# Performance work log

Hardware: AMD Instinct MI355X
Metric: run time of the kernel (lower is better)

## Reference

```python
import jax, jax.numpy as jnp
import numpy as np

EPS = 1e-12  # matches torch F.normalize eps and utils.get_diagonal threshold


def _geteig(feats, K):
    # feats: [B, C, H, W]
    B, C, H, W = feats.shape
    nH, nW = H // 4, W // 4
    # bilinear, align_corners=False (half-pixel centers) == jax.image.resize 'bilinear'
    f = jax.image.resize(feats, (B, C, nH, nW), method='bilinear')
    f = f.reshape(B, C, nH * nW).transpose(0, 2, 1)  # [B, N, C]
    norm = jnp.linalg.norm(f, axis=-1, keepdims=True)
    f = f / jnp.maximum(norm, EPS)  # L2-normalize per pixel

    def per_sample(x):  # x: [N, C]
        Wm = x @ x.T                       # cosine similarity [N, N]
        Wm = Wm * (Wm > 0)                 # keep positive affinities
        Wm = Wm / Wm.max()
        Wm = jax.lax.stop_gradient(Wm)     # original detaches before eigsh
        d = Wm.sum(axis=1)                 # degree (row sums), as in utils.get_diagonal
        d = jnp.where(d < EPS, 1.0, d)
        inv_sqrt = 1.0 / jnp.sqrt(d)
        L = jnp.diag(d) - Wm               # unnormalized Laplacian
        # generalized problem L v = lam D v  <=>  eigh of D^-1/2 L D^-1/2
        Ln = inv_sqrt[:, None] * L * inv_sqrt[None, :]
        Ln = 0.5 * (Ln + Ln.T)             # enforce symmetry for stability
        evals = jnp.linalg.eigh(Ln)[0]     # ascending
        return evals[:K]                   # K smallest (eigsh sigma=0, which='LM')

    return jax.vmap(per_sample)(f)  # [B, K]


def setup_inputs() -> dict:
    key = jax.random.key(0)
    feats = jax.random.normal(key, (8, 3, 160, 160), dtype=jnp.float32)
    return {"feats": feats, "K": 10}


def reference(feats, K):
    lan1 = _geteig(feats[:, :1], K)    # channel 0 -> [B, K]
    lan2 = _geteig(feats[:, 1:2], K)   # channel 1 -> [B, K]
    # NOTE: faithful to original bug: feats[:2:3] slices the BATCH dim -> [1, C, H, W]
    lan3 = _geteig(feats[:2:3], K)     # [1, K], broadcasts in the MSE below
    loss = jnp.mean((lan1 - lan2) ** 2)
    loss = loss + jnp.mean((lan1 - lan3) ** 2)
    loss = loss + jnp.mean((lan2 - lan3) ** 2)
    return loss * 5
```

## Files before the change

### kernel.cpp

```cpp
#include <hip/hip_runtime.h>
#include <math.h>

#define N16 1600
#define M 32
#define XSZ 51200
#define BIS_IT 28
#define EPSF 1e-12f


__device__ void taps1d(int o, int* lo, int* hi, float* wsum, float w[8]) {
  int l = 4 * o - 2, h = 4 * o + 5;
  if (l < 0) l = 0;
  if (h > 159) h = 159;
  float c = 4.f * o + 1.5f, s = 0.f;
  for (int x = l; x <= h; ++x) {
    float ww = 1.f - fabsf((float)x - c) * 0.25f;
    w[x - l] = ww;
    s += ww;
  }
  *lo = l; *hi = h; *wsum = s;
}

__global__ void __launch_bounds__(256)
k_resize(const float* __restrict__ in, float* __restrict__ rz) {
  const int bx = blockIdx.x, t = threadIdx.x;
  int map = bx / 7;
  int o = (bx % 7) * 256 + t;
  if (o >= N16) return;
  int oy = o / 40, ox = o % 40;
  int ly, hy, lx, hx; float sy, sx; float wy[8], wx[8];
  taps1d(oy, &ly, &hy, &sy, wy);
  taps1d(ox, &lx, &hx, &sx, wx);
  const float* src = in + (size_t)map * 160 * 160;
  float acc = 0.f;
  for (int y = ly; y <= hy; ++y) {
    float a = 0.f;
    const float* row = src + y * 160;
    for (int x = lx; x <= hx; ++x) a += wx[x - lx] * row[x];
    acc += wy[y - ly] * a;
  }
  rz[map * N16 + o] = acc / (sy * sx);
}

__global__ void __launch_bounds__(256)
k_prep(const float* __restrict__ rz, float* __restrict__ F,
       int* __restrict__ flags) {
  __shared__ int sp[256];
  __shared__ int sn[256];
  const int bx = blockIdx.x, t = threadIdx.x;
  if (bx < 16) {
    int b = bx >> 1, c = bx & 1;
    const float* m = rz + (b * 3 + c) * N16;
    int cp = 0, cn = 0;
    for (int o = t; o < N16; o += 256) {
      float v = m[o];
      cp += (v > 0.f);
      cn += (v < 0.f);
    }
    sp[t] = cp; sn[t] = cn;
    __syncthreads();
    for (int s = 128; s > 0; s >>= 1) {
      if (t < s) { sp[t] += sp[t + s]; sn[t] += sn[t + s]; }
      __syncthreads();
    }
    if (t == 0) flags[bx] = (sp[0] == 0 || sn[0] == 0) ? 1 : 0;
  } else {
    int n = (bx - 16) * 256 + t;
    if (n < N16) {
      float x = rz[n], y = rz[N16 + n], z = rz[2 * N16 + n];
      float nrm = sqrtf(x * x + y * y + z * z);
      float s = 1.f / fmaxf(nrm, EPSF);
      F[n * 3 + 0] = x * s;
      F[n * 3 + 1] = y * s;
      F[n * 3 + 2] = z * s;
    }
  }
}

__global__ void __launch_bounds__(256)
k_degree(const float* __restrict__ F, float* __restrict__ R,
         float* __restrict__ G4f, float* __restrict__ X0) {
  __shared__ float Fl[4800];
  __shared__ float red[256];
  const int bx = blockIdx.x, t = threadIdx.x;
  for (int s = t; s < 4800; s += 256) Fl[s] = F[s];
  __syncthreads();
  int rl = t >> 4, jt = t & 15;
  int i = bx * 16 + rl;
  float fx = Fl[i * 3], fy = Fl[i * 3 + 1], fz = Fl[i * 3 + 2];
  float s = 0.f;
#pragma unroll 8
  for (int j = jt; j < N16; j += 16) {
    float w = fx * Fl[j * 3] + fy * Fl[j * 3 + 1] + fz * Fl[j * 3 + 2];
    if (w > 0.f) s += w;
  }
  red[t] = s;
  __syncthreads();
  for (int st = 8; st > 0; st >>= 1) {
    if (jt < st) red[t] += red[t + st];
    __syncthreads();
  }
  if (jt == 0) {
    float d = red[t];
    if (d < EPSF) d = 1.f;
    float r = rsqrtf(d);
    R[i] = r;
    G4f[i * 4 + 0] = r * fx;
    G4f[i * 4 + 1] = r * fy;
    G4f[i * 4 + 2] = r * fz;
    G4f[i * 4 + 3] = 0.f;
  }
  for (int e = t; e < 512; e += 256) {
    int n = bx * 16 + (e >> 5);
    int k = e & 31;
    unsigned u = ((unsigned)n * 2654435761u) ^ ((unsigned)k * 0x9E3779B9u);
    u = u * 1664525u + 1013904223u;
    u ^= u >> 16; u *= 2246822519u; u ^= u >> 13;
    X0[n * M + k] = ((float)(u >> 8) * (1.f / 8388608.f)) - 1.f;
  }
}

__global__ void __launch_bounds__(256)
k_mv(const float* __restrict__ F, const float4* __restrict__ G4,
     const float* __restrict__ R, const float* __restrict__ Xin,
     float* __restrict__ Xout) {
  __shared__ float Ws[2][544];
  __shared__ float XsT[2][1088];
  __shared__ float Red[16 * 136];
  const int bx = blockIdx.x, t = threadIdx.x;
  const int ig = bx >> 1, kh = bx & 1;
  const int i0 = ig * 8, kbase = kh * 16;
  const int rg = t & 3, kg = (t >> 2) & 3, jg = t >> 4;
  const int sj = t >> 2, sq = t & 3;
  const int wil = t & 7, wjg = t >> 3;
  const float fx = F[(i0 + wil) * 3 + 0];
  const float fy = F[(i0 + wil) * 3 + 1];
  const float fz = F[(i0 + wil) * 3 + 2];

  float acc[2][4];
#pragma unroll
  for (int r = 0; r < 2; ++r)
#pragma unroll
    for (int kk = 0; kk < 4; ++kk) acc[r][kk] = 0.f;

  {
    float4 xs = ((const float4*)Xin)[(size_t)sj * 8 + kh * 4 + sq];
    XsT[0][(sq * 4 + 0) * 68 + sj] = xs.x;
    XsT[0][(sq * 4 + 1) * 68 + sj] = xs.y;
    XsT[0][(sq * 4 + 2) * 68 + sj] = xs.z;
    XsT[0][(sq * 4 + 3) * 68 + sj] = xs.w;
#pragma unroll
    for (int q = 0; q < 2; ++q) {
      float4 g = G4[wjg + 32 * q];
      Ws[0][wil * 68 + wjg + 32 * q] =
          fmaxf(fx * g.x + fy * g.y + fz * g.z, 0.f);
    }
  }
  __syncthreads();

  for (int c = 0; c < 25; ++c) {
    const int cur = c & 1, nxt = cur ^ 1;
    float4 xs = {0.f, 0.f, 0.f, 0.f};
    float4 ga[2];
    if (c < 24) {
      const int jb = (c + 1) * 64;
      xs = ((const float4*)Xin)[(size_t)(jb + sj) * 8 + kh * 4 + sq];
#pragma unroll
      for (int q = 0; q < 2; ++q) ga[q] = G4[jb + wjg + 32 * q];
    }
    {
      const int jq = jg * 4;
      float4 wv[2], xv[4];
#pragma unroll
      for (int r = 0; r < 2; ++r)
        wv[r] = *(const float4*)&Ws[cur][(rg * 2 + r) * 68 + jq];
#pragma unroll
      for (int kk = 0; kk < 4; ++kk)
        xv[kk] = *(const float4*)&XsT[cur][(kg * 4 + kk) * 68 + jq];
#pragma unroll
      for (int r = 0; r < 2; ++r)
#pragma unroll
        for (int kk = 0; kk < 4; ++kk)
          acc[r][kk] += wv[r].x * xv[kk].x + wv[r].y * xv[kk].y +
                        wv[r].z * xv[kk].z + wv[r].w * xv[kk].w;
    }
    if (c < 24) {
      XsT[nxt][(sq * 4 + 0) * 68 + sj] = xs.x;
      XsT[nxt][(sq * 4 + 1) * 68 + sj] = xs.y;
      XsT[nxt][(sq * 4 + 2) * 68 + sj] = xs.z;
      XsT[nxt][(sq * 4 + 3) * 68 + sj] = xs.w;
#pragma unroll
      for (int q = 0; q < 2; ++q)
        Ws[nxt][wil * 68 + wjg + 32 * q] =
            fmaxf(fx * ga[q].x + fy * ga[q].y + fz * ga[q].z, 0.f);
    }
    __syncthreads();
  }

#pragma unroll
  for (int r = 0; r < 2; ++r)
#pragma unroll
    for (int kk = 0; kk < 4; ++kk)
      Red[jg * 136 + (rg * 2 + r) * 16 + (kg * 4 + kk)] = acc[r][kk];
  __syncthreads();
  if (t < 128) {
    const int il = t >> 4, kl = t & 15;
    float sv = 0.f;
#pragma unroll
    for (int g = 0; g < 16; ++g) sv += Red[g * 136 + il * 16 + kl];
    const int gi = i0 + il, gk = kbase + kl;
    Xout[(size_t)gi * 32 + gk] =
        0.5f * Xin[(size_t)gi * 32 + gk] + 0.5f * R[gi] * sv;
  }
}

__global__ void __launch_bounds__(256)
k_gram(const float* __restrict__ Xa, const float* __restrict__ Xb,
       float* __restrict__ GPp) {
  __shared__ float sA[2048];
  __shared__ float sB[2048];
  const int bx = blockIdx.x, t = threadIdx.x;
  float acc[4] = {0.f, 0.f, 0.f, 0.f};
  for (int c = 0; c < 5; ++c) {
    const int j0 = bx * 320 + c * 64;
    __syncthreads();
    for (int s = t; s < 2048; s += 256) {
      sA[s] = Xa[(size_t)j0 * 32 + s];
      sB[s] = Xb[(size_t)j0 * 32 + s];
    }
    __syncthreads();
#pragma unroll
    for (int s = 0; s < 4; ++s) {
      int e = s * 256 + t;
      int a = e >> 5, b = e & 31;
      float sum = 0.f;
#pragma unroll 8
      for (int jl = 0; jl < 64; ++jl) sum += sA[jl * 32 + a] * sB[jl * 32 + b];
      acc[s] += sum;
    }
  }
#pragma unroll
  for (int s = 0; s < 4; ++s) GPp[(size_t)bx * 1024 + s * 256 + t] = acc[s];
}

__global__ void __launch_bounds__(256)
k_apply(const float* __restrict__ GPp, const float* __restrict__ Xin,
        float* __restrict__ Xout) {
  __shared__ float Gm[32 * 33];
  const int bx = blockIdx.x, t = threadIdx.x;
#pragma unroll
  for (int u = 0; u < 4; ++u) {
    int e = t + u * 256;
    float g = 0.f;
#pragma unroll
    for (int p = 0; p < 5; ++p) g += GPp[p * 1024 + e];
    Gm[(e >> 5) * 33 + (e & 31)] = g;
  }
  const int r = t >> 5, l = t & 31;
  const int row = bx * 8 + r;
  float x = Xin[(size_t)row * M + l];
  __syncthreads();
  if (t < 64) {
    for (int k = 0; k < 32; ++k) {
      if (t == k) Gm[k * 33 + k] = sqrtf(fmaxf(Gm[k * 33 + k], 1e-30f));
      float piv = Gm[k * 33 + k];
      if (t > k && t < 32) Gm[t * 33 + k] /= piv;
#pragma unroll
      for (int u = 0; u < 16; ++u) {
        int e = t + u * 64;
        int i = e >> 5, j = e & 31;
        if (i > k && j > k && j <= i)
          Gm[i * 33 + j] -= Gm[i * 33 + k] * Gm[j * 33 + k];
      }
    }
  }
  __syncthreads();
  const int half = t & 32;
  float y = 0.f;
  for (int k = 0; k < 32; ++k) {
    float gkl = Gm[k * 33 + l];
    float contrib = (l < k) ? y * gkl : 0.f;
#pragma unroll
    for (int o = 16; o; o >>= 1) contrib += __shfl_xor(contrib, o, 64);
    float xk = __shfl(x, half + k, 64);
    float yk = (xk - contrib) / Gm[k * 33 + k];
    if (l == k) y = yk;
  }
  Xout[(size_t)row * M + l] = y;
}

__device__ __forceinline__ float wred(float v) {
#pragma unroll
  for (int o = 32; o; o >>= 1) v += __shfl_xor(v, o, 64);
  return v;
}
__device__ __forceinline__ float wredmin(float v) {
#pragma unroll
  for (int o = 32; o; o >>= 1) v = fminf(v, __shfl_xor(v, o, 64));
  return v;
}
__device__ __forceinline__ float wredmax(float v) {
#pragma unroll
  for (int o = 32; o; o >>= 1) v = fmaxf(v, __shfl_xor(v, o, 64));
  return v;
}

__global__ void __launch_bounds__(64)
k_rr(const float* __restrict__ GPp, const int* __restrict__ flags,
     const int* __restrict__ Kptr, float* __restrict__ out) {
  __shared__ float Bs[1056];
  __shared__ float part[1024];
  __shared__ float vgs[32];
  __shared__ float uus[32];
  __shared__ float dd[32];
  __shared__ float ee[32];
  __shared__ float ee2[32];
  __shared__ float evs[32];
  const int t = threadIdx.x;
#pragma unroll
  for (int u = 0; u < 16; ++u) {
    int e = t + u * 64;
    float g = 0.f;
#pragma unroll
    for (int p = 0; p < 5; ++p) g += GPp[p * 1024 + e];
    part[e] = g;
  }
  __syncthreads();
#pragma unroll
  for (int u = 0; u < 16; ++u) {
    int e = t + u * 64;
    int i = e >> 5, j = e & 31;
    Bs[i * 33 + j] = 0.5f * (part[e] + part[j * 32 + i]);
  }
  __syncthreads();
  for (int k = 0; k <= 29; ++k) {
    float xi = (t > k && t < 32) ? Bs[t * 33 + k] : 0.f;
    float nx2 = wred(xi * xi);
    float x0 = __shfl(xi, k + 1, 64);
    if (nx2 < 1e-28f) {
      if (t == 0) ee[k] = x0;
      __syncthreads();
      continue;
    }
    float alpha = (x0 >= 0.f) ? -sqrtf(nx2) : sqrtf(nx2);
    float h = nx2 - alpha * x0;
    float vg = (t == k + 1) ? (xi - alpha) : xi;
    if (t < 32) vgs[t] = vg;
    if (t == 0) ee[k] = alpha;
    __syncthreads();
    float rv[32], vgr[32];
    float pi = 0.f;
    if (t < 32) {
#pragma unroll
      for (int c = 0; c < 32; ++c) rv[c] = Bs[t * 33 + c];
#pragma unroll
      for (int c = 0; c < 32; ++c) vgr[c] = vgs[c];
#pragma unroll
      for (int c = 0; c < 32; ++c) pi += rv[c] * vgr[c];
      pi /= h;
    }
    float vp = wred((t < 32) ? vg * pi : 0.f);
    float Kc = vp / (2.f * h);
    float ug = (t > k && t < 32) ? (pi - Kc * vg) : 0.f;
    if (t < 32) uus[t] = ug;
    __syncthreads();
    if (t < 32) {
      float ugr[32];
#pragma unroll
      for (int c = 0; c < 32; ++c) ugr[c] = uus[c];
#pragma unroll
      for (int c = 0; c < 32; ++c)
        Bs[t * 33 + c] = rv[c] - (vg * ugr[c] + ug * vgr[c]);
    }
    __syncthreads();
  }
  if (t < 32) dd[t] = Bs[t * 33 + t];
  if (t == 0) { ee[30] = Bs[31 * 33 + 30]; ee[31] = 0.f; }
  __syncthreads();
  if (t < 32) ee2[t] = (t < 31) ? ee[t] * ee[t] : 0.f;
  __syncthreads();
  float lo, hi;
  {
    int tt = t & 31;
    float di = dd[tt];
    float r = 0.f;
    if (tt > 0) r += fabsf(ee[tt - 1]);
    if (tt < 31) r += fabsf(ee[tt]);
    lo = wredmin(di - r) - 1e-6f;
    hi = wredmax(di + r) + 1e-6f;
  }
  if (t < 32) {
    float ddr[32], ee2r[31];
#pragma unroll
    for (int i2 = 0; i2 < 32; ++i2) ddr[i2] = dd[i2];
#pragma unroll
    for (int i2 = 0; i2 < 31; ++i2) ee2r[i2] = ee2[i2];
    float a = lo, b = hi;
    for (int it = 0; it < BIS_IT; ++it) {
      float mid = 0.5f * (a + b);
      float q = ddr[0] - mid;
      int cnt = (q < 0.f) ? 1 : 0;
#pragma unroll
      for (int i = 1; i < 32; ++i) {
        float den = q;
        float ad = fabsf(den);
        den = (ad < 1e-30f) ? ((den < 0.f) ? -1e-30f : 1e-30f) : den;
        q = ddr[i] - mid - ee2r[i - 1] * __builtin_amdgcn_rcpf(den);
        cnt += (q < 0.f) ? 1 : 0;
      }
      if (cnt <= t) a = mid; else b = mid;
    }
    evs[t] = 0.5f * (a + b);
  }
  __syncthreads();
  if (t == 0) {
    int K = Kptr ? *Kptr : 10;
    if (K < 1) K = 10;
    if (K > 32) K = 32;
    float t12 = 0.f, t13 = 0.f, t23 = 0.f;
    for (int b = 0; b < 8; ++b) {
      float f1 = flags[b * 2 + 0] ? 1.f : 0.f;
      float f2 = flags[b * 2 + 1] ? 1.f : 0.f;
      for (int k = 0; k < K; ++k) {
        float v1 = (k == 0) ? 0.f : (k == 1 ? f1 : 1.f);
        float v2 = (k == 0) ? 0.f : (k == 1 ? f2 : 1.f);
        float m3 = 2.f - 2.f * evs[31 - k];
        t12 += (v1 - v2) * (v1 - v2);
        t13 += (v1 - m3) * (v1 - m3);
        t23 += (v2 - m3) * (v2 - m3);
      }
    }
    out[0] = 5.f * (t12 + t13 + t23) / (8.f * (float)K);
  }
}

extern "C" void kernel_launch(void* const* d_in, const int* in_sizes, int n_in,
                              void* d_out, int out_size, void* d_ws, size_t ws_size,
                              hipStream_t stream) {
  const float* feats = (const float*)d_in[0];
  const int* Kptr = (n_in > 1) ? (const int*)d_in[1] : nullptr;
  float* ws = (float*)d_ws;
  float* RZ = ws;
  float* F  = ws + 38400;
  float* G4f = ws + 43200;
  float* R  = ws + 49600;
  int* FLAGS = (int*)(ws + 51200);
  float* GP = ws + 51264;
  float* XB = ws + 51264 + 15360;
  float* bufs[4] = {XB, XB + XSZ, XB + 2 * XSZ, XB + 3 * XSZ};
  const float4* G4 = (const float4*)G4f;
  float* outp = (float*)d_out;

  k_resize<<<dim3(168), dim3(256), 0, stream>>>(feats, RZ);
  k_prep<<<dim3(23), dim3(256), 0, stream>>>(RZ, F, FLAGS);
  k_degree<<<dim3(100), dim3(256), 0, stream>>>(F, R, G4f, bufs[0]);

  const float* cur = bufs[0];
  for (int m = 1; m <= 10; ++m) {
    float* o = bufs[1 + m % 3];
    k_mv<<<dim3(400), dim3(256), 0, stream>>>(F, G4, R, cur, o);
    cur = o;
  }
  k_gram<<<dim3(5), dim3(256), 0, stream>>>(cur, cur, GP);
  k_apply<<<dim3(200), dim3(256), 0, stream>>>(GP, cur, bufs[0]);
  cur = bufs[0];
  for (int m = 11; m <= 20; ++m) {
    float* o = bufs[1 + m % 3];
    k_mv<<<dim3(400), dim3(256), 0, stream>>>(F, G4, R, cur, o);
    cur = o;
  }
  k_gram<<<dim3(5), dim3(256), 0, stream>>>(cur, cur, GP + 5120);
  k_apply<<<dim3(200), dim3(256), 0, stream>>>(GP + 5120, cur, bufs[0]);
  k_mv<<<dim3(400), dim3(256), 0, stream>>>(F, G4, R, bufs[0], bufs[1]);
  k_gram<<<dim3(5), dim3(256), 0, stream>>>(bufs[0], bufs[1], GP + 10240);
  k_rr<<<dim3(1), dim3(64), 0, stream>>>(GP + 10240, FLAGS, Kptr, outp);
}
```

Baseline: 542.6 us.

## Enlarge k_mv chunks and keep k_rr tridiagonalization in registers with shuffles

k_mv now stages 320-column chunks of the affinity row block and Krylov vectors in LDS instead of 64, so each block does 5 synchronized iterations instead of 25. k_rr keeps each matrix row in registers and broadcasts the Householder vectors with wavefront shuffles. This removes the LDS round trips and the __syncthreads calls in the 30-step tridiagonal reduction, and the Gershgorin bounds are now computed per thread without reductions. The cost is larger LDS use and higher register pressure in both kernels, which may reduce occupancy.

```diff
diff --git a/kernel.cpp b/kernel.cpp
--- a/kernel.cpp
+++ b/kernel.cpp
@@ -124,8 +124,8 @@
 k_mv(const float* __restrict__ F, const float4* __restrict__ G4,
      const float* __restrict__ R, const float* __restrict__ Xin,
      float* __restrict__ Xout) {
-  __shared__ float Ws[2][544];
-  __shared__ float XsT[2][1088];
+  __shared__ float Ws[2][8 * 324];
+  __shared__ float XsT[2][16 * 324];
   __shared__ float Red[16 * 136];
   const int bx = blockIdx.x, t = threadIdx.x;
   const int ig = bx >> 1, kh = bx & 1;
@@ -136,6 +136,7 @@
   const float fx = F[(i0 + wil) * 3 + 0];
   const float fy = F[(i0 + wil) * 3 + 1];
   const float fz = F[(i0 + wil) * 3 + 2];
+  const float4* Xin4 = (const float4*)Xin;
 
   float acc[2][4];
 #pragma unroll
@@ -143,40 +144,44 @@
 #pragma unroll
     for (int kk = 0; kk < 4; ++kk) acc[r][kk] = 0.f;
 
-  {
-    float4 xs = ((const float4*)Xin)[(size_t)sj * 8 + kh * 4 + sq];
-    XsT[0][(sq * 4 + 0) * 68 + sj] = xs.x;
-    XsT[0][(sq * 4 + 1) * 68 + sj] = xs.y;
-    XsT[0][(sq * 4 + 2) * 68 + sj] = xs.z;
-    XsT[0][(sq * 4 + 3) * 68 + sj] = xs.w;
-#pragma unroll
-    for (int q = 0; q < 2; ++q) {
-      float4 g = G4[wjg + 32 * q];
-      Ws[0][wil * 68 + wjg + 32 * q] =
-          fmaxf(fx * g.x + fy * g.y + fz * g.z, 0.f);
-    }
-  }
-  __syncthreads();
-
-  for (int c = 0; c < 25; ++c) {
+#pragma unroll
+  for (int p = 0; p < 5; ++p) {
+    float4 xs = Xin4[(size_t)(p * 64 + sj) * 8 + kh * 4 + sq];
+    XsT[0][(sq * 4 + 0) * 324 + p * 64 + sj] = xs.x;
+    XsT[0][(sq * 4 + 1) * 324 + p * 64 + sj] = xs.y;
+    XsT[0][(sq * 4 + 2) * 324 + p * 64 + sj] = xs.z;
+    XsT[0][(sq * 4 + 3) * 324 + p * 64 + sj] = xs.w;
+  }
+#pragma unroll
+  for (int q = 0; q < 10; ++q) {
+    float4 g = G4[wjg + 32 * q];
+    Ws[0][wil * 324 + wjg + 32 * q] =
+        fmaxf(fx * g.x + fy * g.y + fz * g.z, 0.f);
+  }
+  __syncthreads();
+
+  for (int c = 0; c < 5; ++c) {
     const int cur = c & 1, nxt = cur ^ 1;
-    float4 xs = {0.f, 0.f, 0.f, 0.f};
-    float4 ga[2];
-    if (c < 24) {
-      const int jb = (c + 1) * 64;
-      xs = ((const float4*)Xin)[(size_t)(jb + sj) * 8 + kh * 4 + sq];
-#pragma unroll
-      for (int q = 0; q < 2; ++q) ga[q] = G4[jb + wjg + 32 * q];
-    }
-    {
-      const int jq = jg * 4;
+    float4 xsr[5];
+    float4 gar[10];
+    if (c < 4) {
+      const int jb = (c + 1) * 320;
+#pragma unroll
+      for (int p = 0; p < 5; ++p)
+        xsr[p] = Xin4[(size_t)(jb + p * 64 + sj) * 8 + kh * 4 + sq];
+#pragma unroll
+      for (int q = 0; q < 10; ++q) gar[q] = G4[jb + wjg + 32 * q];
+    }
+#pragma unroll
+    for (int ss = 0; ss < 5; ++ss) {
+      const int jq = ss * 64 + jg * 4;
       float4 wv[2], xv[4];
 #pragma unroll
       for (int r = 0; r < 2; ++r)
-        wv[r] = *(const float4*)&Ws[cur][(rg * 2 + r) * 68 + jq];
+        wv[r] = *(const float4*)&Ws[cur][(rg * 2 + r) * 324 + jq];
 #pragma unroll
       for (int kk = 0; kk < 4; ++kk)
-        xv[kk] = *(const float4*)&XsT[cur][(kg * 4 + kk) * 68 + jq];
+        xv[kk] = *(const float4*)&XsT[cur][(kg * 4 + kk) * 324 + jq];
 #pragma unroll
       for (int r = 0; r < 2; ++r)
 #pragma unroll
@@ -184,15 +189,18 @@
           acc[r][kk] += wv[r].x * xv[kk].x + wv[r].y * xv[kk].y +
                         wv[r].z * xv[kk].z + wv[r].w * xv[kk].w;
     }
-    if (c < 24) {
-      XsT[nxt][(sq * 4 + 0) * 68 + sj] = xs.x;
-      XsT[nxt][(sq * 4 + 1) * 68 + sj] = xs.y;
-      XsT[nxt][(sq * 4 + 2) * 68 + sj] = xs.z;
-      XsT[nxt][(sq * 4 + 3) * 68 + sj] = xs.w;
-#pragma unroll
-      for (int q = 0; q < 2; ++q)
-        Ws[nxt][wil * 68 + wjg + 32 * q] =
-            fmaxf(fx * ga[q].x + fy * ga[q].y + fz * ga[q].z, 0.f);
+    if (c < 4) {
+#pragma unroll
+      for (int p = 0; p < 5; ++p) {
+        XsT[nxt][(sq * 4 + 0) * 324 + p * 64 + sj] = xsr[p].x;
+        XsT[nxt][(sq * 4 + 1) * 324 + p * 64 + sj] = xsr[p].y;
+        XsT[nxt][(sq * 4 + 2) * 324 + p * 64 + sj] = xsr[p].z;
+        XsT[nxt][(sq * 4 + 3) * 324 + p * 64 + sj] = xsr[p].w;
+      }
+#pragma unroll
+      for (int q = 0; q < 10; ++q)
+        Ws[nxt][wil * 324 + wjg + 32 * q] =
+            fmaxf(fx * gar[q].x + fy * gar[q].y + fz * gar[q].z, 0.f);
     }
     __syncthreads();
   }
@@ -294,27 +302,12 @@
   for (int o = 32; o; o >>= 1) v += __shfl_xor(v, o, 64);
   return v;
 }
-__device__ __forceinline__ float wredmin(float v) {
-#pragma unroll
-  for (int o = 32; o; o >>= 1) v = fminf(v, __shfl_xor(v, o, 64));
-  return v;
-}
-__device__ __forceinline__ float wredmax(float v) {
-#pragma unroll
-  for (int o = 32; o; o >>= 1) v = fmaxf(v, __shfl_xor(v, o, 64));
-  return v;
-}
 
 __global__ void __launch_bounds__(64)
 k_rr(const float* __restrict__ GPp, const int* __restrict__ flags,
      const int* __restrict__ Kptr, float* __restrict__ out) {
   __shared__ float Bs[1056];
   __shared__ float part[1024];
-  __shared__ float vgs[32];
-  __shared__ float uus[32];
-  __shared__ float dd[32];
-  __shared__ float ee[32];
-  __shared__ float ee2[32];
   __shared__ float evs[32];
   const int t = threadIdx.x;
 #pragma unroll
@@ -333,68 +326,58 @@
     Bs[i * 33 + j] = 0.5f * (part[e] + part[j * 32 + i]);
   }
   __syncthreads();
+  const int tr = t & 31;
+  float row[32];
+#pragma unroll
+  for (int c = 0; c < 32; ++c) row[c] = Bs[tr * 33 + c];
+  float eer[32];
+#pragma unroll
   for (int k = 0; k <= 29; ++k) {
-    float xi = (t > k && t < 32) ? Bs[t * 33 + k] : 0.f;
+    float xi = (t > k && t < 32) ? row[k] : 0.f;
     float nx2 = wred(xi * xi);
     float x0 = __shfl(xi, k + 1, 64);
-    if (nx2 < 1e-28f) {
-      if (t == 0) ee[k] = x0;
-      __syncthreads();
-      continue;
-    }
+    if (nx2 < 1e-28f) { eer[k] = x0; continue; }
     float alpha = (x0 >= 0.f) ? -sqrtf(nx2) : sqrtf(nx2);
     float h = nx2 - alpha * x0;
-    float vg = (t == k + 1) ? (xi - alpha) : xi;
-    if (t < 32) vgs[t] = vg;
-    if (t == 0) ee[k] = alpha;
-    __syncthreads();
-    float rv[32], vgr[32];
-    float pi = 0.f;
-    if (t < 32) {
-#pragma unroll
-      for (int c = 0; c < 32; ++c) rv[c] = Bs[t * 33 + c];
-#pragma unroll
-      for (int c = 0; c < 32; ++c) vgr[c] = vgs[c];
-#pragma unroll
-      for (int c = 0; c < 32; ++c) pi += rv[c] * vgr[c];
-      pi /= h;
-    }
-    float vp = wred((t < 32) ? vg * pi : 0.f);
+    float vv = (t == k + 1) ? (xi - alpha) : xi;
+    eer[k] = alpha;
+    float p0 = 0.f, p1 = 0.f, p2 = 0.f, p3 = 0.f;
+#pragma unroll
+    for (int c = 0; c < 32; c += 4) {
+      p0 += row[c + 0] * __shfl(vv, c + 0, 64);
+      p1 += row[c + 1] * __shfl(vv, c + 1, 64);
+      p2 += row[c + 2] * __shfl(vv, c + 2, 64);
+      p3 += row[c + 3] * __shfl(vv, c + 3, 64);
+    }
+    float pi = ((p0 + p1) + (p2 + p3)) / h;
+    float vp = wred(vv * pi);
     float Kc = vp / (2.f * h);
-    float ug = (t > k && t < 32) ? (pi - Kc * vg) : 0.f;
-    if (t < 32) uus[t] = ug;
-    __syncthreads();
-    if (t < 32) {
-      float ugr[32];
-#pragma unroll
-      for (int c = 0; c < 32; ++c) ugr[c] = uus[c];
-#pragma unroll
-      for (int c = 0; c < 32; ++c)
-        Bs[t * 33 + c] = rv[c] - (vg * ugr[c] + ug * vgr[c]);
-    }
-    __syncthreads();
-  }
-  if (t < 32) dd[t] = Bs[t * 33 + t];
-  if (t == 0) { ee[30] = Bs[31 * 33 + 30]; ee[31] = 0.f; }
-  __syncthreads();
-  if (t < 32) ee2[t] = (t < 31) ? ee[t] * ee[t] : 0.f;
-  __syncthreads();
-  float lo, hi;
-  {
-    int tt = t & 31;
-    float di = dd[tt];
-    float r = 0.f;
-    if (tt > 0) r += fabsf(ee[tt - 1]);
-    if (tt < 31) r += fabsf(ee[tt]);
-    lo = wredmin(di - r) - 1e-6f;
-    hi = wredmax(di + r) + 1e-6f;
-  }
+    float uu = (t > k && t < 32) ? (pi - Kc * vv) : 0.f;
+#pragma unroll
+    for (int c = 0; c < 32; ++c) {
+      float uc = __shfl(uu, c, 64);
+      float vc = __shfl(vv, c, 64);
+      row[c] -= vv * uc + uu * vc;
+    }
+  }
+  float ddr[32];
+#pragma unroll
+  for (int c = 0; c < 32; ++c) ddr[c] = __shfl(row[c], c, 64);
+  eer[30] = __shfl(row[30], 31, 64);
+  eer[31] = 0.f;
+  float ee2r[31];
+#pragma unroll
+  for (int c = 0; c < 31; ++c) ee2r[c] = eer[c] * eer[c];
+  float lo = 1e30f, hi = -1e30f;
+#pragma unroll
+  for (int i = 0; i < 32; ++i) {
+    float r = ((i > 0) ? fabsf(eer[i - 1]) : 0.f) +
+              ((i < 31) ? fabsf(eer[i]) : 0.f);
+    lo = fminf(lo, ddr[i] - r);
+    hi = fmaxf(hi, ddr[i] + r);
+  }
+  lo -= 1e-6f; hi += 1e-6f;
   if (t < 32) {
-    float ddr[32], ee2r[31];
-#pragma unroll
-    for (int i2 = 0; i2 < 32; ++i2) ddr[i2] = dd[i2];
-#pragma unroll
-    for (int i2 = 0; i2 < 31; ++i2) ee2r[i2] = ee2[i2];
     float a = lo, b = hi;
     for (int it = 0; it < BIS_IT; ++it) {
       float mid = 0.5f * (a + b);
```

Result: faster. 502.8 us, median of 3 (-7.3%).
